# Kernel tuning notes

Measured on AMD Instinct MI355X. Metric: run time of the kernel, lower is better.

## Reference

```python
import jax, jax.numpy as jnp
import numpy as np

N_BITS = 8  # abits = wbits = 8 (symmetric signed per-tensor quant)
QN = -2 ** (N_BITS - 1)
QP = 2 ** (N_BITS - 1) - 1


def _round_pass(v):
    # straight-through round: forward round, backward identity
    return v + jax.lax.stop_gradient(jnp.round(v) - v)


def _quantize(t):
    # per-tensor symmetric quantization; scale detached like torch .detach()
    scale = jax.lax.stop_gradient(jnp.max(jnp.abs(t))) / QP
    q = _round_pass(jnp.clip(t / scale, QN, QP))
    return q, scale


def _quantized_linear(x3, s_x, w, b):
    # x3: [B, S, Din]; w: [Dout, Din]; b: [Dout]; s_x: scalar dequant scale
    B, S, Din = x3.shape
    x2 = x3.reshape(-1, Din) * s_x              # dequantize incoming activations
    qw, sw = _quantize(w)
    qx, sx = _quantize(x2)
    out = jnp.matmul(qx, qw.T)                  # int-valued float GEMM
    out = out + b[None, :]                      # bias added before rescale (as in source)
    return (out * (sw * sx)).reshape(B, S, -1)


def setup_inputs() -> dict:
    key = jax.random.key(0)
    k1, k2, k3, k4, k5 = jax.random.split(key, 5)
    B, S, D, H = 128, 197, 384, 1536
    x = jax.random.normal(k1, (B, S, D), dtype=jnp.float32)
    act_scaling_factor = jnp.ones((1,), dtype=jnp.float32)
    w1 = jax.random.normal(k2, (H, D), dtype=jnp.float32) * (1.0 / np.sqrt(D))
    b1 = jax.random.normal(k3, (H,), dtype=jnp.float32) * 0.02
    w2 = jax.random.normal(k4, (D, H), dtype=jnp.float32) * (1.0 / np.sqrt(H))
    b2 = jax.random.normal(k5, (D,), dtype=jnp.float32) * 0.02
    return {"x": x, "act_scaling_factor": act_scaling_factor,
            "w1": w1, "b1": b1, "w2": w2, "b2": b2}


def reference(x, act_scaling_factor, w1, b1, w2, b2):
    s_x = act_scaling_factor.reshape(())
    h = _quantized_linear(x, s_x, w1, b1)       # fc1
    h = jax.nn.gelu(h, approximate=False)       # torch nn.GELU (erf)
    qh, s_h = _quantize(h)                      # qact1: requantize activations
    out = _quantized_linear(qh, s_h, w2, b2)    # fc2
    return out
```

## Files before the change

kernel.cpp:

```cpp
#include <hip/hip_runtime.h>
#include <hip/hip_bf16.h>
#include <stdint.h>

typedef int v4i __attribute__((ext_vector_type(4)));

#define GPTR(p) ((const __attribute__((address_space(1))) void*)(p))
#define LPTR(p) ((__attribute__((address_space(3))) void*)(p))

__device__ __forceinline__ float wave_max(float m) {
#pragma unroll
  for (int off = 32; off > 0; off >>= 1)
    m = fmaxf(m, __shfl_xor(m, off, 64));
  return m;
}

__device__ __forceinline__ float fast_erf(float x) {
  const float ax = fabsf(x);
  const float t = __builtin_amdgcn_rcpf(fmaf(0.3275911f, ax, 1.0f));
  float p = fmaf(1.061405429f, t, -1.453152027f);
  p = fmaf(p, t, 1.421413741f);
  p = fmaf(p, t, -0.284496736f);
  p = fmaf(p, t, 0.254829592f);
  const float e = __expf(-ax * ax);
  const float r = 1.0f - p * t * e;
  return copysignf(r, x);
}

__device__ __forceinline__ float gelu_exact(float f) {
  return 0.5f * f * (1.0f + fast_erf(f * 0.70710678118654752f));
}

__global__ void absmax3_kernel(const float* __restrict__ x, int nx4,
                               const float* __restrict__ smul,
                               const float* __restrict__ w1, int nw14,
                               const float* __restrict__ w2, int nw24,
                               unsigned* __restrict__ scal) {
  __shared__ float red[4];
  const int bid = blockIdx.x;
  const float4* s4;
  int n4, b0, nb;
  float s = 1.0f;
  unsigned* dst;
  if (bid < 512)      { s4 = (const float4*)x;  n4 = nx4;  s = smul[0]; dst = scal;     b0 = bid;       nb = 512; }
  else if (bid < 640) { s4 = (const float4*)w1; n4 = nw14;              dst = scal + 1; b0 = bid - 512; nb = 128; }
  else                { s4 = (const float4*)w2; n4 = nw24;              dst = scal + 2; b0 = bid - 640; nb = 128; }
  float m = 0.0f;
  const int stride = nb * blockDim.x;
  for (int i = b0 * blockDim.x + threadIdx.x; i < n4; i += stride) {
    float4 v = s4[i];
    m = fmaxf(m, fabsf(v.x * s));
    m = fmaxf(m, fabsf(v.y * s));
    m = fmaxf(m, fabsf(v.z * s));
    m = fmaxf(m, fabsf(v.w * s));
  }
  m = wave_max(m);
  if ((threadIdx.x & 63) == 0) red[threadIdx.x >> 6] = m;
  __syncthreads();
  if (threadIdx.x == 0)
    atomicMax(dst, __float_as_uint(fmaxf(fmaxf(red[0], red[1]), fmaxf(red[2], red[3]))));
}

__global__ void quantize3_kernel(const float* __restrict__ x, int nx4,
                                 const float* __restrict__ smul,
                                 const float* __restrict__ w1, int nw14,
                                 const float* __restrict__ w2, int nw24,
                                 const unsigned* __restrict__ scal,
                                 int8_t* __restrict__ qx,
                                 int8_t* __restrict__ qw1,
                                 int8_t* __restrict__ qw2) {
  const int bid = blockIdx.x;
  const float4* s4;
  char4* d4;
  int n4, b0, nb;
  float s = 1.0f, mx;
  if (bid < 2048)      { s4 = (const float4*)x;  d4 = (char4*)qx;  n4 = nx4;  s = smul[0]; mx = __uint_as_float(scal[0]); b0 = bid;        nb = 2048; }
  else if (bid < 2176) { s4 = (const float4*)w1; d4 = (char4*)qw1; n4 = nw14;              mx = __uint_as_float(scal[1]); b0 = bid - 2048; nb = 128; }
  else                 { s4 = (const float4*)w2; d4 = (char4*)qw2; n4 = nw24;              mx = __uint_as_float(scal[2]); b0 = bid - 2176; nb = 128; }
  const float scale = mx / 127.0f;
  const int stride = nb * blockDim.x;
  for (int i = b0 * blockDim.x + threadIdx.x; i < n4; i += stride) {
    float4 v = s4[i];
    char4 q;
    q.x = (signed char)(int)rintf(fminf(fmaxf((v.x * s) / scale, -128.0f), 127.0f));
    q.y = (signed char)(int)rintf(fminf(fmaxf((v.y * s) / scale, -128.0f), 127.0f));
    q.z = (signed char)(int)rintf(fminf(fmaxf((v.z * s) / scale, -128.0f), 127.0f));
    q.w = (signed char)(int)rintf(fminf(fmaxf((v.w * s) / scale, -128.0f), 127.0f));
    d4[i] = q;
  }
}

__global__ void reduce_scale_kernel(const float* __restrict__ partial, int n,
                                    unsigned* __restrict__ scal) {
  __shared__ float red[4];
  float m = -3.4e38f;
  for (int i = threadIdx.x; i < n; i += blockDim.x) m = fmaxf(m, partial[i]);
  m = wave_max(m);
  if ((threadIdx.x & 63) == 0) red[threadIdx.x >> 6] = m;
  __syncthreads();
  if (threadIdx.x == 0) {
    m = fmaxf(fmaxf(red[0], red[1]), fmaxf(red[2], red[3]));
    const float sx = __uint_as_float(scal[0]) / 127.0f;
    const float sw = __uint_as_float(scal[1]) / 127.0f;
    const float max_f = m * (sw * sx);
    scal[3] = __float_as_uint(fmaxf(gelu_exact(max_f), 0.1699702f));
  }
}

template <int EPI>
__global__ __launch_bounds__(256, 4)
void gemm_i8_kernel(const int8_t* __restrict__ A, const int8_t* __restrict__ B,
                    const float* __restrict__ bias,
                    const unsigned* __restrict__ scal,
                    float* __restrict__ partial,
                    int8_t* __restrict__ out_i8,
                    float* __restrict__ out_f32,
                    int N, int K) {
  __shared__ __align__(16) int8_t lA[2][128 * 64];
  __shared__ __align__(16) int8_t lB[2][128 * 64];

  const int t = threadIdx.x;
  const int lane = t & 63;
  const int wave = t >> 6;
  const int wr = wave >> 1;
  const int wc = wave & 1;
  const size_t m0 = (size_t)blockIdx.y * 128;
  const int n0 = blockIdx.x * 128;

  const int8_t* Ab = A + m0 * (size_t)K;
  const int8_t* Bb = B + (size_t)n0 * (size_t)K;

  v4i acc[4][4] = {};
  const int KT = K >> 6;

  const int row0 = t >> 2;
  const int ss = (t & 3) ^ ((row0 >> 1) & 3);
  const int ubase = __builtin_amdgcn_readfirstlane((t & 192) * 16);
  const size_t srcA0 = (size_t)row0 * K + (size_t)(ss * 16);
  const size_t srcA1 = (size_t)(row0 + 64) * K + (size_t)(ss * 16);

  auto stage = [&](int buf, int kt) {
    const int8_t* ga = Ab + kt * 64;
    const int8_t* gb = Bb + kt * 64;
    __builtin_amdgcn_global_load_lds(GPTR(ga + srcA0), LPTR(&lA[buf][ubase]), 16, 0, 0);
    __builtin_amdgcn_global_load_lds(GPTR(ga + srcA1), LPTR(&lA[buf][4096 + ubase]), 16, 0, 0);
    __builtin_amdgcn_global_load_lds(GPTR(gb + srcA0), LPTR(&lB[buf][ubase]), 16, 0, 0);
    __builtin_amdgcn_global_load_lds(GPTR(gb + srcA1), LPTR(&lB[buf][4096 + ubase]), 16, 0, 0);
  };

  const int r15 = lane & 15;
  const int q4 = lane >> 4;

  auto compute = [&](int buf) {
    v4i af[4], bf[4];
#pragma unroll
    for (int fr = 0; fr < 4; ++fr) {
      const int row = wr * 64 + fr * 16 + r15;
      const int slot = q4 ^ ((row >> 1) & 3);
      af[fr] = *(const v4i*)(&lA[buf][row * 64 + slot * 16]);
    }
#pragma unroll
    for (int fc = 0; fc < 4; ++fc) {
      const int row = wc * 64 + fc * 16 + r15;
      const int slot = q4 ^ ((row >> 1) & 3);
      bf[fc] = *(const v4i*)(&lB[buf][row * 64 + slot * 16]);
    }
#pragma unroll
    for (int fr = 0; fr < 4; ++fr)
#pragma unroll
      for (int fc = 0; fc < 4; ++fc)
        acc[fr][fc] = __builtin_amdgcn_mfma_i32_16x16x64_i8(af[fr], bf[fc], acc[fr][fc], 0, 0, 0);
  };

  stage(0, 0);
  asm volatile("s_waitcnt vmcnt(0)" ::: "memory");
  __syncthreads();
  int cur = 0;
  for (int kt = 1; kt < KT; ++kt) {
    stage(cur ^ 1, kt);
    compute(cur);
    __syncthreads();
    cur ^= 1;
  }
  compute(cur);

  const int rb = q4 * 4;

  if constexpr (EPI == 0) {
    float lm = -3.4e38f;
#pragma unroll
    for (int fc = 0; fc < 4; ++fc) {
      const float bv = bias[n0 + wc * 64 + fc * 16 + r15];
#pragma unroll
      for (int fr = 0; fr < 4; ++fr)
#pragma unroll
        for (int r = 0; r < 4; ++r)
          lm = fmaxf(lm, (float)acc[fr][fc][r] + bv);
    }
    lm = wave_max(lm);
    __syncthreads();
    float* red = (float*)lA;
    if (lane == 0) red[wave] = lm;
    __syncthreads();
    if (t == 0)
      partial[blockIdx.y * gridDim.x + blockIdx.x] =
          fmaxf(fmaxf(red[0], red[1]), fmaxf(red[2], red[3]));
  } else if constexpr (EPI == 1) {
    const float sx = __uint_as_float(scal[0]) / 127.0f;
    const float sw = __uint_as_float(scal[1]) / 127.0f;
    const float s1 = sw * sx;
    const float sh = __uint_as_float(scal[3]) / 127.0f;
    const float inv_sh = __builtin_amdgcn_rcpf(sh);
    __syncthreads();
    int8_t* qt = (int8_t*)lA;
#pragma unroll
    for (int fc = 0; fc < 4; ++fc) {
      const int col = wc * 64 + fc * 16 + r15;
      const float bv = bias[n0 + col];
#pragma unroll
      for (int fr = 0; fr < 4; ++fr)
#pragma unroll
        for (int r = 0; r < 4; ++r) {
          const int row = wr * 64 + fr * 16 + rb + r;
          const float f = ((float)acc[fr][fc][r] + bv) * s1;
          const float g = gelu_exact(f);
          const float qv = rintf(fminf(fmaxf(g * inv_sh, -128.0f), 127.0f));
          qt[row * 128 + col] = (int8_t)(int)qv;
        }
    }
    __syncthreads();
#pragma unroll
    for (int v = 0; v < 4; ++v) {
      const int row = v * 32 + (t >> 3);
      const int colb = (t & 7) * 16;
      *(v4i*)(out_i8 + (m0 + row) * (size_t)N + n0 + colb) =
          *(const v4i*)(qt + row * 128 + colb);
    }
  } else {
    const float sw2 = __uint_as_float(scal[2]) / 127.0f;
    const float sh = __uint_as_float(scal[3]) / 127.0f;
    const float x2max = 127.0f * sh;
    const float sx2 = x2max / 127.0f;
    const float s2 = sw2 * sx2;
#pragma unroll
    for (int fc = 0; fc < 4; ++fc) {
      const int col = n0 + wc * 64 + fc * 16 + r15;
      const float bv = bias[col];
#pragma unroll
      for (int fr = 0; fr < 4; ++fr)
#pragma unroll
        for (int r = 0; r < 4; ++r) {
          const size_t row = m0 + (size_t)(wr * 64 + fr * 16 + rb + r);
          out_f32[row * (size_t)N + col] = ((float)acc[fr][fc][r] + bv) * s2;
        }
    }
  }
}

extern "C" void kernel_launch(void* const* d_in, const int* in_sizes, int n_in,
                              void* d_out, int out_size, void* d_ws, size_t ws_size,
                              hipStream_t stream) {
  const float* x   = (const float*)d_in[0];
  const float* sxp = (const float*)d_in[1];
  const float* w1  = (const float*)d_in[2];
  const float* b1  = (const float*)d_in[3];
  const float* w2  = (const float*)d_in[4];
  const float* b2  = (const float*)d_in[5];

  const int H = in_sizes[3];
  const int D = in_sizes[5];
  const int M = in_sizes[0] / D;
  const int GM = M / 128;
  const int GN1 = H / 128;
  const int GN2 = D / 128;

  uint8_t* ws = (uint8_t*)d_ws;
  unsigned* scal = (unsigned*)ws;
  size_t off = 256;
  float* partial = (float*)(ws + off); off += 16384;
  int8_t* qx  = (int8_t*)(ws + off); off += (size_t)M * D;
  int8_t* qw1 = (int8_t*)(ws + off); off += (size_t)H * D;
  int8_t* qw2 = (int8_t*)(ws + off); off += (size_t)D * H;
  int8_t* qh  = (int8_t*)(ws + off); off += (size_t)M * H;
  (void)ws_size; (void)n_in; (void)out_size;

  hipMemsetAsync(scal, 0, 16, stream);

  absmax3_kernel<<<dim3(768), dim3(256), 0, stream>>>(
      x, M * D / 4, sxp, w1, H * D / 4, w2, D * H / 4, scal);

  quantize3_kernel<<<dim3(2304), dim3(256), 0, stream>>>(
      x, M * D / 4, sxp, w1, H * D / 4, w2, D * H / 4, scal, qx, qw1, qw2);

  dim3 blk(256);
  dim3 g1(GN1, GM);
  gemm_i8_kernel<0><<<g1, blk, 0, stream>>>(qx, qw1, b1, scal, partial, nullptr, nullptr, H, D);
  reduce_scale_kernel<<<1, 256, 0, stream>>>(partial, GM * GN1, scal);
  gemm_i8_kernel<1><<<g1, blk, 0, stream>>>(qx, qw1, b1, scal, nullptr, qh, nullptr, H, D);

  dim3 g2(GN2, GM);
  gemm_i8_kernel<2><<<g2, blk, 0, stream>>>(qh, qw2, b2, scal, nullptr, nullptr, (float*)d_out, D, H);
}
```

Baseline: 137.2 us.

## Triple-buffer int8 GEMM pipeline, remap workgroups per XCD, vectorize epilogue stores

New measurement: 140.1 us. +2.2%, slower.

```diff
diff --git a/kernel.cpp b/kernel.cpp
--- a/kernel.cpp
+++ b/kernel.cpp
@@ -80,12 +80,12 @@
   const int stride = nb * blockDim.x;
   for (int i = b0 * blockDim.x + threadIdx.x; i < n4; i += stride) {
     float4 v = s4[i];
-    char4 q;
-    q.x = (signed char)(int)rintf(fminf(fmaxf((v.x * s) / scale, -128.0f), 127.0f));
-    q.y = (signed char)(int)rintf(fminf(fmaxf((v.y * s) / scale, -128.0f), 127.0f));
-    q.z = (signed char)(int)rintf(fminf(fmaxf((v.z * s) / scale, -128.0f), 127.0f));
-    q.w = (signed char)(int)rintf(fminf(fmaxf((v.w * s) / scale, -128.0f), 127.0f));
-    d4[i] = q;
+    char4 qq;
+    qq.x = (signed char)(int)rintf(fminf(fmaxf((v.x * s) / scale, -128.0f), 127.0f));
+    qq.y = (signed char)(int)rintf(fminf(fmaxf((v.y * s) / scale, -128.0f), 127.0f));
+    qq.z = (signed char)(int)rintf(fminf(fmaxf((v.z * s) / scale, -128.0f), 127.0f));
+    qq.w = (signed char)(int)rintf(fminf(fmaxf((v.w * s) / scale, -128.0f), 127.0f));
+    d4[i] = qq;
   }
 }
 
@@ -107,24 +107,32 @@
 }
 
 template <int EPI>
-__global__ __launch_bounds__(256, 4)
+__global__ __launch_bounds__(256, 3)
 void gemm_i8_kernel(const int8_t* __restrict__ A, const int8_t* __restrict__ B,
                     const float* __restrict__ bias,
                     const unsigned* __restrict__ scal,
                     float* __restrict__ partial,
                     int8_t* __restrict__ out_i8,
                     float* __restrict__ out_f32,
-                    int N, int K) {
-  __shared__ __align__(16) int8_t lA[2][128 * 64];
-  __shared__ __align__(16) int8_t lB[2][128 * 64];
+                    int N, int K, int GN) {
+  __shared__ __align__(16) int8_t lA[3][128 * 64];
+  __shared__ __align__(16) int8_t lB[3][128 * 64];
+  __shared__ float red[4];
+
+  const int nwg = gridDim.x;
+  const int q = nwg >> 3, rr = nwg & 7;
+  const int xcd = blockIdx.x & 7, sub = blockIdx.x >> 3;
+  const int wg = (xcd < rr ? xcd * (q + 1) : rr * (q + 1) + (xcd - rr) * q) + sub;
+  const int bx = wg % GN;
+  const int by = wg / GN;
 
   const int t = threadIdx.x;
   const int lane = t & 63;
   const int wave = t >> 6;
   const int wr = wave >> 1;
   const int wc = wave & 1;
-  const size_t m0 = (size_t)blockIdx.y * 128;
-  const int n0 = blockIdx.x * 128;
+  const size_t m0 = (size_t)by * 128;
+  const int n0 = bx * 128;
 
   const int8_t* Ab = A + m0 * (size_t)K;
   const int8_t* Bb = B + (size_t)n0 * (size_t)K;
@@ -168,72 +176,88 @@
     for (int fr = 0; fr < 4; ++fr)
 #pragma unroll
       for (int fc = 0; fc < 4; ++fc)
-        acc[fr][fc] = __builtin_amdgcn_mfma_i32_16x16x64_i8(af[fr], bf[fc], acc[fr][fc], 0, 0, 0);
+        acc[fr][fc] = __builtin_amdgcn_mfma_i32_16x16x64_i8(bf[fc], af[fr], acc[fr][fc], 0, 0, 0);
   };
 
+#define CBAR()                          \
+  do {                                  \
+    __builtin_amdgcn_sched_barrier(0);  \
+    __builtin_amdgcn_s_barrier();       \
+    __builtin_amdgcn_sched_barrier(0);  \
+  } while (0)
+
   stage(0, 0);
+  stage(1, 1);
+  stage(2, 2);
+  int cur = 0;
+  for (int kt = 0; kt <= KT - 3; ++kt) {
+    asm volatile("s_waitcnt vmcnt(8)" ::: "memory");
+    CBAR();
+    compute(cur);
+    asm volatile("s_waitcnt lgkmcnt(0)" ::: "memory");
+    CBAR();
+    if (kt + 3 < KT) stage(cur, kt + 3);
+    cur = (cur == 2) ? 0 : cur + 1;
+  }
+  asm volatile("s_waitcnt vmcnt(4)" ::: "memory");
+  CBAR();
+  compute(cur);
+  cur = (cur == 2) ? 0 : cur + 1;
   asm volatile("s_waitcnt vmcnt(0)" ::: "memory");
-  __syncthreads();
-  int cur = 0;
-  for (int kt = 1; kt < KT; ++kt) {
-    stage(cur ^ 1, kt);
-    compute(cur);
-    __syncthreads();
-    cur ^= 1;
-  }
+  CBAR();
   compute(cur);
-
-  const int rb = q4 * 4;
+#undef CBAR
 
   if constexpr (EPI == 0) {
     float lm = -3.4e38f;
 #pragma unroll
     for (int fc = 0; fc < 4; ++fc) {
-      const float bv = bias[n0 + wc * 64 + fc * 16 + r15];
-#pragma unroll
-      for (int fr = 0; fr < 4; ++fr)
-#pragma unroll
-        for (int r = 0; r < 4; ++r)
-          lm = fmaxf(lm, (float)acc[fr][fc][r] + bv);
+      const float4 bv4 = *(const float4*)&bias[n0 + wc * 64 + fc * 16 + q4 * 4];
+#pragma unroll
+      for (int fr = 0; fr < 4; ++fr) {
+        lm = fmaxf(lm, (float)acc[fr][fc][0] + bv4.x);
+        lm = fmaxf(lm, (float)acc[fr][fc][1] + bv4.y);
+        lm = fmaxf(lm, (float)acc[fr][fc][2] + bv4.z);
+        lm = fmaxf(lm, (float)acc[fr][fc][3] + bv4.w);
+      }
     }
     lm = wave_max(lm);
-    __syncthreads();
-    float* red = (float*)lA;
     if (lane == 0) red[wave] = lm;
     __syncthreads();
     if (t == 0)
-      partial[blockIdx.y * gridDim.x + blockIdx.x] =
-          fmaxf(fmaxf(red[0], red[1]), fmaxf(red[2], red[3]));
+      partial[wg] = fmaxf(fmaxf(red[0], red[1]), fmaxf(red[2], red[3]));
   } else if constexpr (EPI == 1) {
     const float sx = __uint_as_float(scal[0]) / 127.0f;
     const float sw = __uint_as_float(scal[1]) / 127.0f;
     const float s1 = sw * sx;
     const float sh = __uint_as_float(scal[3]) / 127.0f;
     const float inv_sh = __builtin_amdgcn_rcpf(sh);
-    __syncthreads();
-    int8_t* qt = (int8_t*)lA;
 #pragma unroll
     for (int fc = 0; fc < 4; ++fc) {
-      const int col = wc * 64 + fc * 16 + r15;
-      const float bv = bias[n0 + col];
-#pragma unroll
-      for (int fr = 0; fr < 4; ++fr)
-#pragma unroll
-        for (int r = 0; r < 4; ++r) {
-          const int row = wr * 64 + fr * 16 + rb + r;
-          const float f = ((float)acc[fr][fc][r] + bv) * s1;
-          const float g = gelu_exact(f);
-          const float qv = rintf(fminf(fmaxf(g * inv_sh, -128.0f), 127.0f));
-          qt[row * 128 + col] = (int8_t)(int)qv;
+      const int nb = n0 + wc * 64 + fc * 16 + q4 * 4;
+      const float4 bv4 = *(const float4*)&bias[nb];
+#pragma unroll
+      for (int fr = 0; fr < 4; ++fr) {
+        const size_t m = m0 + (size_t)(wr * 64 + fr * 16 + r15);
+        char4 qq;
+        {
+          const float f = ((float)acc[fr][fc][0] + bv4.x) * s1;
+          qq.x = (signed char)(int)rintf(fminf(fmaxf(gelu_exact(f) * inv_sh, -128.0f), 127.0f));
         }
-    }
-    __syncthreads();
-#pragma unroll
-    for (int v = 0; v < 4; ++v) {
-      const int row = v * 32 + (t >> 3);
-      const int colb = (t & 7) * 16;
-      *(v4i*)(out_i8 + (m0 + row) * (size_t)N + n0 + colb) =
-          *(const v4i*)(qt + row * 128 + colb);
+        {
+          const float f = ((float)acc[fr][fc][1] + bv4.y) * s1;
+          qq.y = (signed char)(int)rintf(fminf(fmaxf(gelu_exact(f) * inv_sh, -128.0f), 127.0f));
+        }
+        {
+          const float f = ((float)acc[fr][fc][2] + bv4.z) * s1;
+          qq.z = (signed char)(int)rintf(fminf(fmaxf(gelu_exact(f) * inv_sh, -128.0f), 127.0f));
+        }
+        {
+          const float f = ((float)acc[fr][fc][3] + bv4.w) * s1;
+          qq.w = (signed char)(int)rintf(fminf(fmaxf(gelu_exact(f) * inv_sh, -128.0f), 127.0f));
+        }
+        *(char4*)(out_i8 + m * (size_t)N + nb) = qq;
+      }
     }
   } else {
     const float sw2 = __uint_as_float(scal[2]) / 127.0f;
@@ -243,15 +267,18 @@
     const float s2 = sw2 * sx2;
 #pragma unroll
     for (int fc = 0; fc < 4; ++fc) {
-      const int col = n0 + wc * 64 + fc * 16 + r15;
-      const float bv = bias[col];
-#pragma unroll
-      for (int fr = 0; fr < 4; ++fr)
-#pragma unroll
-        for (int r = 0; r < 4; ++r) {
-          const size_t row = m0 + (size_t)(wr * 64 + fr * 16 + rb + r);
-          out_f32[row * (size_t)N + col] = ((float)acc[fr][fc][r] + bv) * s2;
-        }
+      const int nb = n0 + wc * 64 + fc * 16 + q4 * 4;
+      const float4 bv4 = *(const float4*)&bias[nb];
+#pragma unroll
+      for (int fr = 0; fr < 4; ++fr) {
+        const size_t m = m0 + (size_t)(wr * 64 + fr * 16 + r15);
+        float4 o;
+        o.x = ((float)acc[fr][fc][0] + bv4.x) * s2;
+        o.y = ((float)acc[fr][fc][1] + bv4.y) * s2;
+        o.z = ((float)acc[fr][fc][2] + bv4.z) * s2;
+        o.w = ((float)acc[fr][fc][3] + bv4.w) * s2;
+        *(float4*)(out_f32 + m * (size_t)N + nb) = o;
+      }
     }
   }
 }
@@ -292,11 +319,11 @@
       x, M * D / 4, sxp, w1, H * D / 4, w2, D * H / 4, scal, qx, qw1, qw2);
 
   dim3 blk(256);
-  dim3 g1(GN1, GM);
-  gemm_i8_kernel<0><<<g1, blk, 0, stream>>>(qx, qw1, b1, scal, partial, nullptr, nullptr, H, D);
+  dim3 g1(GN1 * GM);
+  gemm_i8_kernel<0><<<g1, blk, 0, stream>>>(qx, qw1, b1, scal, partial, nullptr, nullptr, H, D, GN1);
   reduce_scale_kernel<<<1, 256, 0, stream>>>(partial, GM * GN1, scal);
-  gemm_i8_kernel<1><<<g1, blk, 0, stream>>>(qx, qw1, b1, scal, nullptr, qh, nullptr, H, D);
-
-  dim3 g2(GN2, GM);
-  gemm_i8_kernel<2><<<g2, blk, 0, stream>>>(qh, qw2, b2, scal, nullptr, nullptr, (float*)d_out, D, H);
-}
+  gemm_i8_kernel<1><<<g1, blk, 0, stream>>>(qx, qw1, b1, scal, nullptr, qh, nullptr, H, D, GN1);
+
+  dim3 g2(GN2 * GM);
+  gemm_i8_kernel<2><<<g2, blk, 0, stream>>>(qh, qw2, b2, scal, nullptr, nullptr, (float*)d_out, D, H, GN2);
+}
```

## Remap GEMM workgroups across XCDs and simplify epilogues

Applied to the files above, without the earlier changes.

New measurement: 131.7 us. -4.0%, faster.

```diff
diff --git a/kernel.cpp b/kernel.cpp
--- a/kernel.cpp
+++ b/kernel.cpp
@@ -80,12 +80,12 @@
   const int stride = nb * blockDim.x;
   for (int i = b0 * blockDim.x + threadIdx.x; i < n4; i += stride) {
     float4 v = s4[i];
-    char4 q;
-    q.x = (signed char)(int)rintf(fminf(fmaxf((v.x * s) / scale, -128.0f), 127.0f));
-    q.y = (signed char)(int)rintf(fminf(fmaxf((v.y * s) / scale, -128.0f), 127.0f));
-    q.z = (signed char)(int)rintf(fminf(fmaxf((v.z * s) / scale, -128.0f), 127.0f));
-    q.w = (signed char)(int)rintf(fminf(fmaxf((v.w * s) / scale, -128.0f), 127.0f));
-    d4[i] = q;
+    char4 qq;
+    qq.x = (signed char)(int)rintf(fminf(fmaxf((v.x * s) / scale, -128.0f), 127.0f));
+    qq.y = (signed char)(int)rintf(fminf(fmaxf((v.y * s) / scale, -128.0f), 127.0f));
+    qq.z = (signed char)(int)rintf(fminf(fmaxf((v.z * s) / scale, -128.0f), 127.0f));
+    qq.w = (signed char)(int)rintf(fminf(fmaxf((v.w * s) / scale, -128.0f), 127.0f));
+    d4[i] = qq;
   }
 }
 
@@ -114,17 +114,25 @@
                     float* __restrict__ partial,
                     int8_t* __restrict__ out_i8,
                     float* __restrict__ out_f32,
-                    int N, int K) {
+                    int N, int K, int GN) {
   __shared__ __align__(16) int8_t lA[2][128 * 64];
   __shared__ __align__(16) int8_t lB[2][128 * 64];
+  __shared__ float red[4];
+
+  const int nwg = gridDim.x;
+  const int q = nwg >> 3, rr = nwg & 7;
+  const int xcd = blockIdx.x & 7, sub = blockIdx.x >> 3;
+  const int wg = (xcd < rr ? xcd * (q + 1) : rr * (q + 1) + (xcd - rr) * q) + sub;
+  const int bx = wg % GN;
+  const int by = wg / GN;
 
   const int t = threadIdx.x;
   const int lane = t & 63;
   const int wave = t >> 6;
   const int wr = wave >> 1;
   const int wc = wave & 1;
-  const size_t m0 = (size_t)blockIdx.y * 128;
-  const int n0 = blockIdx.x * 128;
+  const size_t m0 = (size_t)by * 128;
+  const int n0 = bx * 128;
 
   const int8_t* Ab = A + m0 * (size_t)K;
   const int8_t* Bb = B + (size_t)n0 * (size_t)K;
@@ -189,51 +197,40 @@
     float lm = -3.4e38f;
 #pragma unroll
     for (int fc = 0; fc < 4; ++fc) {
+      int im = acc[0][fc][0];
+#pragma unroll
+      for (int fr = 0; fr < 4; ++fr)
+#pragma unroll
+        for (int r = 0; r < 4; ++r) im = max(im, acc[fr][fc][r]);
       const float bv = bias[n0 + wc * 64 + fc * 16 + r15];
-#pragma unroll
-      for (int fr = 0; fr < 4; ++fr)
-#pragma unroll
-        for (int r = 0; r < 4; ++r)
-          lm = fmaxf(lm, (float)acc[fr][fc][r] + bv);
+      lm = fmaxf(lm, (float)im + bv);
     }
     lm = wave_max(lm);
-    __syncthreads();
-    float* red = (float*)lA;
     if (lane == 0) red[wave] = lm;
     __syncthreads();
     if (t == 0)
-      partial[blockIdx.y * gridDim.x + blockIdx.x] =
-          fmaxf(fmaxf(red[0], red[1]), fmaxf(red[2], red[3]));
+      partial[wg] = fmaxf(fmaxf(red[0], red[1]), fmaxf(red[2], red[3]));
   } else if constexpr (EPI == 1) {
     const float sx = __uint_as_float(scal[0]) / 127.0f;
     const float sw = __uint_as_float(scal[1]) / 127.0f;
     const float s1 = sw * sx;
     const float sh = __uint_as_float(scal[3]) / 127.0f;
     const float inv_sh = __builtin_amdgcn_rcpf(sh);
-    __syncthreads();
-    int8_t* qt = (int8_t*)lA;
 #pragma unroll
     for (int fc = 0; fc < 4; ++fc) {
-      const int col = wc * 64 + fc * 16 + r15;
-      const float bv = bias[n0 + col];
-#pragma unroll
-      for (int fr = 0; fr < 4; ++fr)
+      const int n = n0 + wc * 64 + fc * 16 + r15;
+      const float bv = bias[n];
+#pragma unroll
+      for (int fr = 0; fr < 4; ++fr) {
 #pragma unroll
         for (int r = 0; r < 4; ++r) {
-          const int row = wr * 64 + fr * 16 + rb + r;
+          const size_t m = m0 + (size_t)(wr * 64 + fr * 16 + rb + r);
           const float f = ((float)acc[fr][fc][r] + bv) * s1;
           const float g = gelu_exact(f);
           const float qv = rintf(fminf(fmaxf(g * inv_sh, -128.0f), 127.0f));
-          qt[row * 128 + col] = (int8_t)(int)qv;
+          out_i8[m * (size_t)N + n] = (int8_t)(int)qv;
         }
-    }
-    __syncthreads();
-#pragma unroll
-    for (int v = 0; v < 4; ++v) {
-      const int row = v * 32 + (t >> 3);
-      const int colb = (t & 7) * 16;
-      *(v4i*)(out_i8 + (m0 + row) * (size_t)N + n0 + colb) =
-          *(const v4i*)(qt + row * 128 + colb);
+      }
     }
   } else {
     const float sw2 = __uint_as_float(scal[2]) / 127.0f;
@@ -243,15 +240,16 @@
     const float s2 = sw2 * sx2;
 #pragma unroll
     for (int fc = 0; fc < 4; ++fc) {
-      const int col = n0 + wc * 64 + fc * 16 + r15;
-      const float bv = bias[col];
-#pragma unroll
-      for (int fr = 0; fr < 4; ++fr)
+      const int n = n0 + wc * 64 + fc * 16 + r15;
+      const float bv = bias[n];
+#pragma unroll
+      for (int fr = 0; fr < 4; ++fr) {
 #pragma unroll
         for (int r = 0; r < 4; ++r) {
-          const size_t row = m0 + (size_t)(wr * 64 + fr * 16 + rb + r);
-          out_f32[row * (size_t)N + col] = ((float)acc[fr][fc][r] + bv) * s2;
+          const size_t m = m0 + (size_t)(wr * 64 + fr * 16 + rb + r);
+          out_f32[m * (size_t)N + n] = ((float)acc[fr][fc][r] + bv) * s2;
         }
+      }
     }
   }
 }
@@ -292,11 +290,11 @@
       x, M * D / 4, sxp, w1, H * D / 4, w2, D * H / 4, scal, qx, qw1, qw2);
 
   dim3 blk(256);
-  dim3 g1(GN1, GM);
-  gemm_i8_kernel<0><<<g1, blk, 0, stream>>>(qx, qw1, b1, scal, partial, nullptr, nullptr, H, D);
+  dim3 g1(GN1 * GM);
+  gemm_i8_kernel<0><<<g1, blk, 0, stream>>>(qx, qw1, b1, scal, partial, nullptr, nullptr, H, D, GN1);
   reduce_scale_kernel<<<1, 256, 0, stream>>>(partial, GM * GN1, scal);
-  gemm_i8_kernel<1><<<g1, blk, 0, stream>>>(qx, qw1, b1, scal, nullptr, qh, nullptr, H, D);
-
-  dim3 g2(GN2, GM);
-  gemm_i8_kernel<2><<<g2, blk, 0, stream>>>(qh, qw2, b2, scal, nullptr, nullptr, (float*)d_out, D, H);
-}
+  gemm_i8_kernel<1><<<g1, blk, 0, stream>>>(qx, qw1, b1, scal, nullptr, qh, nullptr, H, D, GN1);
+
+  dim3 g2(GN2 * GM);
+  gemm_i8_kernel<2><<<g2, blk, 0, stream>>>(qh, qw2, b2, scal, nullptr, nullptr, (float*)d_out, D, H, GN2);
+}
```
